# Optimization experiments

Measured on AMD Instinct MI355X. Metric: run time of the kernel, lower is better.

## Reference

```python
import jax, jax.numpy as jnp
import numpy as np

B, V, H = 128, 50257, 2048   # batch, vocab, history length
NEG_INF = jnp.float32(-jnp.inf)
TEMP_MIN = 1e-5


def setup_inputs() -> dict:
    key = jax.random.key(0)
    k1, k2, k3 = jax.random.split(key, 3)
    logits = jax.random.normal(k1, (B, V), jnp.float32) * 4.0
    previous_tokens = jax.random.randint(k2, (B, H), 0, V)
    # uniform noise for the exponential-race (Gumbel-max) draw; strictly positive
    u = jax.random.uniform(k3, (B, V), jnp.float32, minval=1e-10, maxval=1.0)
    return {
        "logits": logits,
        "previous_tokens": previous_tokens,
        "u": u,
        "top_p": jnp.full((1,), 0.9, jnp.float32),
        "repetition_penalty": jnp.full((1,), 1.35, jnp.float32),
        "temperature": jnp.full((1,), 0.7, jnp.float32),
        "top_k": 50,
    }


def _logits_to_probs(logits, previous_tokens, temperature, top_k, top_p, repetition_penalty):
    b = jnp.arange(logits.shape[0])[:, None]  # [B,1] row index for scatters
    # repetition penalty: gather history scores, shrink, scatter back
    score = jnp.take_along_axis(logits, previous_tokens, axis=1)          # [B,H]
    score = jnp.where(score < 0, score * repetition_penalty, score / repetition_penalty)
    logits = logits.at[b, previous_tokens].set(score)                     # [B,V]
    # nucleus (top-p) filtering via descending sort + cumulative softmax
    order = jnp.argsort(-logits, axis=-1)                                 # [B,V]
    sorted_logits = jnp.take_along_axis(logits, order, axis=1)
    cum_probs = jnp.cumsum(jax.nn.softmax(sorted_logits, axis=-1), axis=-1)
    remove_sorted = cum_probs > top_p
    remove_sorted = remove_sorted.at[:, 0].set(False)                     # keep best token
    # scatter removal mask back to vocab order (order is a permutation)
    remove = jnp.zeros_like(remove_sorted).at[b, order].set(remove_sorted)
    logits = jnp.where(remove, NEG_INF, logits)
    # temperature + top-k pivot filter
    logits = logits / jnp.maximum(temperature, TEMP_MIN)
    v = jax.lax.top_k(logits, top_k)[0]                                   # [B,top_k]
    pivot = v[:, -1:]
    logits = jnp.where(logits < pivot, NEG_INF, logits)
    return jax.nn.softmax(logits, axis=-1)


def reference(logits, previous_tokens, u, top_p, repetition_penalty, temperature, top_k):
    previous_tokens = previous_tokens.astype(jnp.int32)
    probs = _logits_to_probs(logits, previous_tokens, temperature, top_k, top_p,
                             repetition_penalty)
    # multinomial_sample_one_no_sync: exponential race argmax(probs / Exp(1))
    q = -jnp.log(u)
    idx_next = jnp.argmax(probs / q, axis=-1, keepdims=True).astype(jnp.int32)
    return idx_next, probs
```

## Files before the change

kernel.cpp:

```cpp
#include <hip/hip_runtime.h>
#include <cfloat>
#include <cmath>
#include <cstdint>

#define VV 50257
#define NT 1024
#define NBUCK 4096
#define CAP 1024
#define BITW ((VV + 31) / 32)
#define NW (NT / 64)

__device__ __forceinline__ unsigned fmono(float f) {
    unsigned b = __float_as_uint(f);
    return b ^ (((int)b < 0) ? 0xFFFFFFFFu : 0x80000000u);
}

__global__ __launch_bounds__(NT) void pp_fused(
    const float* __restrict__ logits, const int* __restrict__ prev,
    const float* __restrict__ u, const float* __restrict__ toppp,
    const float* __restrict__ rpp, const float* __restrict__ tempp,
    const int* __restrict__ topkp, float* __restrict__ out_idx,
    float* __restrict__ out_probs, int Hp)
{
    __shared__ unsigned bitmap[BITW];
    __shared__ unsigned hist[NBUCK];
    __shared__ float cand_v[CAP];
    __shared__ int   cand_i[CAP];
    __shared__ float red_m[NW], red_s[NW];
    __shared__ unsigned wtot[NW];
    __shared__ float tv[64];
    __shared__ int   ti[64];
    __shared__ float sM, sS;
    __shared__ int sT, sCnt;

    const int row = blockIdx.x;
    const int tid = threadIdx.x;
    const int lane = tid & 63;
    const int wid = tid >> 6;
    const float rp = rpp[0];
    const float inv_rp = 1.0f / rp;

    for (int i = tid; i < BITW; i += NT) bitmap[i] = 0u;
    for (int i = tid; i < NBUCK; i += NT) hist[i] = 0u;
    if (tid == 0) { sT = 0; sCnt = 0; }
    if (tid < 64) { tv[tid] = -FLT_MAX; ti[tid] = 0x7FFFFFFF; }
    __syncthreads();

    const int* prow = prev + (size_t)row * Hp;
    for (int i = tid; i < Hp; i += NT) {
        int t = prow[i];
        atomicOr(&bitmap[t >> 5], 1u << (t & 31));
    }
    __syncthreads();

    const float* lrow = logits + (size_t)row * VV;
    float* orow = out_probs + (size_t)row * VV;
    const int pad = (4 - (row & 3)) & 3;
    const int n4 = (VV - pad) >> 2;
    const int tail0 = pad + 4 * n4;
    const float4* lrow4 = (const float4*)(lrow + pad);
    float4* orow4 = (float4*)(orow + pad);

    float m = -FLT_MAX;
    if (tid < pad) {
        float l = lrow[tid];
        if ((bitmap[tid >> 5] >> (tid & 31)) & 1u) l = (l < 0.f) ? l * rp : l * inv_rp;
        atomicAdd(&hist[fmono(l) >> 20], 1u);
        m = fmaxf(m, l);
    }
    #pragma unroll 4
    for (int k = tid; k < n4; k += NT) {
        float4 v = lrow4[k];
        const int base = pad + 4 * k;
        float e[4] = {v.x, v.y, v.z, v.w};
        #pragma unroll
        for (int j = 0; j < 4; ++j) {
            int i = base + j;
            float l = e[j];
            if ((bitmap[i >> 5] >> (i & 31)) & 1u) l = (l < 0.f) ? l * rp : l * inv_rp;
            atomicAdd(&hist[fmono(l) >> 20], 1u);
            m = fmaxf(m, l);
        }
    }
    for (int i = tail0 + tid; i < VV; i += NT) {
        float l = lrow[i];
        if ((bitmap[i >> 5] >> (i & 31)) & 1u) l = (l < 0.f) ? l * rp : l * inv_rp;
        atomicAdd(&hist[fmono(l) >> 20], 1u);
        m = fmaxf(m, l);
    }

    if (tid < pad) orow[tid] = 0.0f;
    const float4 z4 = make_float4(0.f, 0.f, 0.f, 0.f);
    for (int k = tid; k < n4; k += NT) orow4[k] = z4;
    for (int i = tail0 + tid; i < VV; i += NT) orow[i] = 0.0f;

    #pragma unroll
    for (int off = 32; off; off >>= 1) m = fmaxf(m, __shfl_down(m, off));
    if (lane == 0) red_m[wid] = m;
    __syncthreads();
    if (tid == 0) {
        float M = red_m[0];
        for (int w = 1; w < NW; ++w) M = fmaxf(M, red_m[w]);
        sM = M;
    }

    unsigned c = hist[tid * 4] + hist[tid * 4 + 1] + hist[tid * 4 + 2] + hist[tid * 4 + 3];
    unsigned v = c;
    #pragma unroll
    for (int off = 1; off < 64; off <<= 1) {
        unsigned o = __shfl_down(v, off);
        if (lane + off < 64) v += o;
    }
    if (lane == 0) wtot[wid] = v;
    __syncthreads();
    unsigned add = 0;
    for (int w = wid + 1; w < NW; ++w) add += wtot[w];
    const unsigned mySuf = v + add;
    const unsigned sufExcl = mySuf - c;
    if (mySuf >= 64u && sufExcl < 64u) {
        unsigned above = sufExcl;
        for (int b = tid * 4 + 3; b >= tid * 4; --b) {
            above += hist[b];
            if (above >= 64u) { sT = b; break; }
        }
    }
    __syncthreads();
    const unsigned T = (unsigned)sT;
    const float M = sM;

    float s = 0.0f;
    if (tid < pad) {
        float l = lrow[tid];
        if ((bitmap[tid >> 5] >> (tid & 31)) & 1u) l = (l < 0.f) ? l * rp : l * inv_rp;
        s += __expf(l - M);
        if ((fmono(l) >> 20) >= T) {
            int p = atomicAdd(&sCnt, 1);
            if (p < CAP) { cand_v[p] = l; cand_i[p] = tid; }
        }
    }
    #pragma unroll 2
    for (int k = tid; k < n4; k += NT) {
        float4 vv = lrow4[k];
        const int base = pad + 4 * k;
        float e[4] = {vv.x, vv.y, vv.z, vv.w};
        #pragma unroll
        for (int j = 0; j < 4; ++j) {
            int i = base + j;
            float l = e[j];
            if ((bitmap[i >> 5] >> (i & 31)) & 1u) l = (l < 0.f) ? l * rp : l * inv_rp;
            s += __expf(l - M);
            if ((fmono(l) >> 20) >= T) {
                int p = atomicAdd(&sCnt, 1);
                if (p < CAP) { cand_v[p] = l; cand_i[p] = i; }
            }
        }
    }
    for (int i = tail0 + tid; i < VV; i += NT) {
        float l = lrow[i];
        if ((bitmap[i >> 5] >> (i & 31)) & 1u) l = (l < 0.f) ? l * rp : l * inv_rp;
        s += __expf(l - M);
        if ((fmono(l) >> 20) >= T) {
            int p = atomicAdd(&sCnt, 1);
            if (p < CAP) { cand_v[p] = l; cand_i[p] = i; }
        }
    }
    #pragma unroll
    for (int off = 32; off; off >>= 1) s += __shfl_down(s, off);
    if (lane == 0) red_s[wid] = s;
    __syncthreads();
    if (tid == 0) {
        float Ss = red_s[0];
        for (int w = 1; w < NW; ++w) Ss += red_s[w];
        sS = Ss;
    }
    const int cnt = min(sCnt, CAP);

    if (tid < cnt) {
        float vi = cand_v[tid]; int ii = cand_i[tid];
        int r = 0;
        for (int j = 0; j < cnt; ++j) {
            float vj = cand_v[j]; int ij = cand_i[j];
            r += (int)((vj > vi) || (vj == vi && ij < ii));
        }
        if (r < 64) { tv[r] = vi; ti[r] = ii; }
    }
    __syncthreads();

    if (tid < 64) {
        const float top_p = toppp[0];
        const float temp = tempp[0];
        int K = topkp[0]; K = min(max(K, 1), 64);
        const float Ssum = sS;
        float vl = tv[lane];
        int ci = ti[lane];
        bool val = (vl > -FLT_MAX);
        bool act = (lane < K) && val;
        float e = act ? expf(vl - M) / Ssum : 0.0f;
        float cum = e;
        #pragma unroll
        for (int off = 1; off < 64; off <<= 1) {
            float pv = __shfl_up(cum, off);
            if (lane >= off) cum += pv;
        }
        unsigned long long bal = __ballot(act && (cum <= top_p));
        int n = (int)__popcll(bal);
        if (n < 1) n = 1;
        const float v0 = tv[0];
        const float invT = 1.0f / fmaxf(temp, 1e-5f);
        bool keep = (lane < n) && val;
        float w = keep ? expf((vl - v0) * invT) : 0.0f;
        float Z = w;
        #pragma unroll
        for (int off = 32; off; off >>= 1) Z += __shfl_xor(Z, off);
        float p = keep ? (w / Z) : 0.0f;
        if (keep) orow[ci] = p;
        float ratio = -1.0f;
        if (keep) ratio = p / (-logf(u[(size_t)row * VV + ci]));
        int bi = keep ? ci : 0x7FFFFFFF;
        #pragma unroll
        for (int off = 32; off; off >>= 1) {
            float orat = __shfl_xor(ratio, off);
            int oidx = __shfl_xor(bi, off);
            if (orat > ratio || (orat == ratio && oidx < bi)) { ratio = orat; bi = oidx; }
        }
        if (lane == 0) out_idx[row] = (float)bi;
    }
}

extern "C" void kernel_launch(void* const* d_in, const int* in_sizes, int n_in,
                              void* d_out, int out_size, void* d_ws, size_t ws_size,
                              hipStream_t stream) {
    const float* logits = (const float*)d_in[0];
    const int*   prev   = (const int*)d_in[1];
    const float* u      = (const float*)d_in[2];
    const float* topp   = (const float*)d_in[3];
    const float* rp     = (const float*)d_in[4];
    const float* temp   = (const float*)d_in[5];
    const int*   topk   = (const int*)d_in[6];

    const int B  = in_sizes[0] / VV;
    const int Hp = in_sizes[1] / B;

    float* out = (float*)d_out;
    pp_fused<<<B, NT, 0, stream>>>(
        logits, prev, u, topp, rp, temp, topk, out, out + B, Hp);
}
```

Baseline: 33.08 us.

## Split each row across four blocks and merge candidates in a second kernel

The single fused kernel with one block per row becomes two kernels. The first runs SPLITS=4 blocks per row, each handling a vocab chunk. Each chunk block builds its own histogram and candidate list, keeps loaded values in registers instead of re-reading logits in the second pass, and writes a partial max, sum and candidates to workspace. The second kernel merges the partial softmax stats, ranks the combined candidates and does top-p/top-k/sampling. This targets low occupancy (only 128 blocks on a many-CU GPU) at the cost of an extra launch and global round trips for candidates.

```diff
diff --git a/kernel.cpp b/kernel.cpp
--- a/kernel.cpp
+++ b/kernel.cpp
@@ -4,95 +4,104 @@
 #include <cstdint>
 
 #define VV 50257
-#define NT 1024
+#define SPLITS 4
+#define CHUNKA 12568
+#define BMW ((CHUNKA + 31) / 32)
 #define NBUCK 4096
-#define CAP 1024
-#define BITW ((VV + 31) / 32)
-#define NW (NT / 64)
+#define CAPC 256
+#define K1T 512
+#define K2T 512
+#define NJ 7
+#define NW1 (K1T / 64)
 
 __device__ __forceinline__ unsigned fmono(float f) {
     unsigned b = __float_as_uint(f);
     return b ^ (((int)b < 0) ? 0xFFFFFFFFu : 0x80000000u);
 }
 
-__global__ __launch_bounds__(NT) void pp_fused(
+__global__ __launch_bounds__(K1T) void pp_k1(
     const float* __restrict__ logits, const int* __restrict__ prev,
-    const float* __restrict__ u, const float* __restrict__ toppp,
-    const float* __restrict__ rpp, const float* __restrict__ tempp,
-    const int* __restrict__ topkp, float* __restrict__ out_idx,
-    float* __restrict__ out_probs, int Hp)
+    const float* __restrict__ rpp,
+    float* __restrict__ pm, float* __restrict__ ps,
+    float* __restrict__ gcv, int* __restrict__ gci, int* __restrict__ gcnt,
+    float* __restrict__ out_probs, int Hp, int capc)
 {
-    __shared__ unsigned bitmap[BITW];
+    const int sp = blockIdx.x, row = blockIdx.y;
+    const int tid = threadIdx.x, lane = tid & 63, wid = tid >> 6;
+    const int c0 = sp * CHUNKA;
+    const int c1 = min(VV, c0 + CHUNKA);
+    const int len = c1 - c0;
+    const float rp = rpp[0], inv_rp = 1.0f / rp;
+
+    __shared__ unsigned bm[BMW];
     __shared__ unsigned hist[NBUCK];
-    __shared__ float cand_v[CAP];
-    __shared__ int   cand_i[CAP];
-    __shared__ float red_m[NW], red_s[NW];
-    __shared__ unsigned wtot[NW];
-    __shared__ float tv[64];
-    __shared__ int   ti[64];
-    __shared__ float sM, sS;
+    __shared__ float red_m[NW1], red_s[NW1];
+    __shared__ unsigned wtot[NW1];
+    __shared__ float cand_v[CAPC];
+    __shared__ int   cand_i[CAPC];
+    __shared__ float sM;
     __shared__ int sT, sCnt;
 
-    const int row = blockIdx.x;
-    const int tid = threadIdx.x;
-    const int lane = tid & 63;
-    const int wid = tid >> 6;
-    const float rp = rpp[0];
-    const float inv_rp = 1.0f / rp;
-
-    for (int i = tid; i < BITW; i += NT) bitmap[i] = 0u;
-    for (int i = tid; i < NBUCK; i += NT) hist[i] = 0u;
+    for (int i = tid; i < BMW; i += K1T) bm[i] = 0u;
+    for (int i = tid; i < NBUCK; i += K1T) hist[i] = 0u;
     if (tid == 0) { sT = 0; sCnt = 0; }
-    if (tid < 64) { tv[tid] = -FLT_MAX; ti[tid] = 0x7FFFFFFF; }
     __syncthreads();
 
     const int* prow = prev + (size_t)row * Hp;
-    for (int i = tid; i < Hp; i += NT) {
+    for (int i = tid; i < Hp; i += K1T) {
         int t = prow[i];
-        atomicOr(&bitmap[t >> 5], 1u << (t & 31));
+        if (t >= c0 && t < c1) {
+            int o = t - c0;
+            atomicOr(&bm[o >> 5], 1u << (o & 31));
+        }
     }
     __syncthreads();
 
     const float* lrow = logits + (size_t)row * VV;
     float* orow = out_probs + (size_t)row * VV;
     const int pad = (4 - (row & 3)) & 3;
-    const int n4 = (VV - pad) >> 2;
+    const int n4 = (len - pad) >> 2;
     const int tail0 = pad + 4 * n4;
-    const float4* lrow4 = (const float4*)(lrow + pad);
-    float4* orow4 = (float4*)(orow + pad);
-
+    const float4* l4 = (const float4*)(lrow + c0 + pad);
+    float4* o4 = (float4*)(orow + c0 + pad);
+
+    float4 rv[NJ];
     float m = -FLT_MAX;
-    if (tid < pad) {
-        float l = lrow[tid];
-        if ((bitmap[tid >> 5] >> (tid & 31)) & 1u) l = (l < 0.f) ? l * rp : l * inv_rp;
+    for (int o = tid; o < pad; o += K1T) {
+        float l = lrow[c0 + o];
+        if ((bm[o >> 5] >> (o & 31)) & 1u) l = (l < 0.f) ? l * rp : l * inv_rp;
         atomicAdd(&hist[fmono(l) >> 20], 1u);
         m = fmaxf(m, l);
     }
-    #pragma unroll 4
-    for (int k = tid; k < n4; k += NT) {
-        float4 v = lrow4[k];
-        const int base = pad + 4 * k;
-        float e[4] = {v.x, v.y, v.z, v.w};
-        #pragma unroll
-        for (int j = 0; j < 4; ++j) {
-            int i = base + j;
-            float l = e[j];
-            if ((bitmap[i >> 5] >> (i & 31)) & 1u) l = (l < 0.f) ? l * rp : l * inv_rp;
-            atomicAdd(&hist[fmono(l) >> 20], 1u);
-            m = fmaxf(m, l);
-        }
-    }
-    for (int i = tail0 + tid; i < VV; i += NT) {
-        float l = lrow[i];
-        if ((bitmap[i >> 5] >> (i & 31)) & 1u) l = (l < 0.f) ? l * rp : l * inv_rp;
+    #pragma unroll
+    for (int j = 0; j < NJ; ++j) {
+        int k = tid + j * K1T;
+        if (k < n4) {
+            float4 v = l4[k];
+            int ob = pad + 4 * k;
+            float x;
+            x = v.x; if ((bm[(ob+0) >> 5] >> ((ob+0) & 31)) & 1u) x = (x < 0.f) ? x * rp : x * inv_rp;
+            atomicAdd(&hist[fmono(x) >> 20], 1u); m = fmaxf(m, x); v.x = x;
+            x = v.y; if ((bm[(ob+1) >> 5] >> ((ob+1) & 31)) & 1u) x = (x < 0.f) ? x * rp : x * inv_rp;
+            atomicAdd(&hist[fmono(x) >> 20], 1u); m = fmaxf(m, x); v.y = x;
+            x = v.z; if ((bm[(ob+2) >> 5] >> ((ob+2) & 31)) & 1u) x = (x < 0.f) ? x * rp : x * inv_rp;
+            atomicAdd(&hist[fmono(x) >> 20], 1u); m = fmaxf(m, x); v.z = x;
+            x = v.w; if ((bm[(ob+3) >> 5] >> ((ob+3) & 31)) & 1u) x = (x < 0.f) ? x * rp : x * inv_rp;
+            atomicAdd(&hist[fmono(x) >> 20], 1u); m = fmaxf(m, x); v.w = x;
+            rv[j] = v;
+        }
+    }
+    for (int o = tail0 + tid; o < len; o += K1T) {
+        float l = lrow[c0 + o];
+        if ((bm[o >> 5] >> (o & 31)) & 1u) l = (l < 0.f) ? l * rp : l * inv_rp;
         atomicAdd(&hist[fmono(l) >> 20], 1u);
         m = fmaxf(m, l);
     }
 
-    if (tid < pad) orow[tid] = 0.0f;
+    for (int o = tid; o < pad; o += K1T) orow[c0 + o] = 0.f;
     const float4 z4 = make_float4(0.f, 0.f, 0.f, 0.f);
-    for (int k = tid; k < n4; k += NT) orow4[k] = z4;
-    for (int i = tail0 + tid; i < VV; i += NT) orow[i] = 0.0f;
+    for (int k = tid; k < n4; k += K1T) o4[k] = z4;
+    for (int o = tail0 + tid; o < len; o += K1T) orow[c0 + o] = 0.f;
 
     #pragma unroll
     for (int off = 32; off; off >>= 1) m = fmaxf(m, __shfl_down(m, off));
@@ -100,11 +109,13 @@
     __syncthreads();
     if (tid == 0) {
         float M = red_m[0];
-        for (int w = 1; w < NW; ++w) M = fmaxf(M, red_m[w]);
+        for (int w = 1; w < NW1; ++w) M = fmaxf(M, red_m[w]);
         sM = M;
     }
 
-    unsigned c = hist[tid * 4] + hist[tid * 4 + 1] + hist[tid * 4 + 2] + hist[tid * 4 + 3];
+    unsigned c = 0;
+    #pragma unroll
+    for (int j = 0; j < 8; ++j) c += hist[tid * 8 + j];
     unsigned v = c;
     #pragma unroll
     for (int off = 1; off < 64; off <<= 1) {
@@ -114,12 +125,12 @@
     if (lane == 0) wtot[wid] = v;
     __syncthreads();
     unsigned add = 0;
-    for (int w = wid + 1; w < NW; ++w) add += wtot[w];
+    for (int w = wid + 1; w < NW1; ++w) add += wtot[w];
     const unsigned mySuf = v + add;
     const unsigned sufExcl = mySuf - c;
     if (mySuf >= 64u && sufExcl < 64u) {
         unsigned above = sufExcl;
-        for (int b = tid * 4 + 3; b >= tid * 4; --b) {
+        for (int b = tid * 8 + 7; b >= tid * 8; --b) {
             above += hist[b];
             if (above >= 64u) { sT = b; break; }
         }
@@ -127,59 +138,110 @@
     __syncthreads();
     const unsigned T = (unsigned)sT;
     const float M = sM;
+    const int cmax = min(capc, CAPC);
 
     float s = 0.0f;
-    if (tid < pad) {
-        float l = lrow[tid];
-        if ((bitmap[tid >> 5] >> (tid & 31)) & 1u) l = (l < 0.f) ? l * rp : l * inv_rp;
+    for (int o = tid; o < pad; o += K1T) {
+        float l = lrow[c0 + o];
+        if ((bm[o >> 5] >> (o & 31)) & 1u) l = (l < 0.f) ? l * rp : l * inv_rp;
         s += __expf(l - M);
         if ((fmono(l) >> 20) >= T) {
             int p = atomicAdd(&sCnt, 1);
-            if (p < CAP) { cand_v[p] = l; cand_i[p] = tid; }
-        }
-    }
-    #pragma unroll 2
-    for (int k = tid; k < n4; k += NT) {
-        float4 vv = lrow4[k];
-        const int base = pad + 4 * k;
-        float e[4] = {vv.x, vv.y, vv.z, vv.w};
-        #pragma unroll
-        for (int j = 0; j < 4; ++j) {
-            int i = base + j;
-            float l = e[j];
-            if ((bitmap[i >> 5] >> (i & 31)) & 1u) l = (l < 0.f) ? l * rp : l * inv_rp;
-            s += __expf(l - M);
-            if ((fmono(l) >> 20) >= T) {
-                int p = atomicAdd(&sCnt, 1);
-                if (p < CAP) { cand_v[p] = l; cand_i[p] = i; }
-            }
-        }
-    }
-    for (int i = tail0 + tid; i < VV; i += NT) {
-        float l = lrow[i];
-        if ((bitmap[i >> 5] >> (i & 31)) & 1u) l = (l < 0.f) ? l * rp : l * inv_rp;
+            if (p < cmax) { cand_v[p] = l; cand_i[p] = c0 + o; }
+        }
+    }
+    #pragma unroll
+    for (int j = 0; j < NJ; ++j) {
+        int k = tid + j * K1T;
+        if (k < n4) {
+            float4 vv = rv[j];
+            int gi = c0 + pad + 4 * k;
+            s += __expf(vv.x - M);
+            if ((fmono(vv.x) >> 20) >= T) { int p = atomicAdd(&sCnt, 1); if (p < cmax) { cand_v[p] = vv.x; cand_i[p] = gi + 0; } }
+            s += __expf(vv.y - M);
+            if ((fmono(vv.y) >> 20) >= T) { int p = atomicAdd(&sCnt, 1); if (p < cmax) { cand_v[p] = vv.y; cand_i[p] = gi + 1; } }
+            s += __expf(vv.z - M);
+            if ((fmono(vv.z) >> 20) >= T) { int p = atomicAdd(&sCnt, 1); if (p < cmax) { cand_v[p] = vv.z; cand_i[p] = gi + 2; } }
+            s += __expf(vv.w - M);
+            if ((fmono(vv.w) >> 20) >= T) { int p = atomicAdd(&sCnt, 1); if (p < cmax) { cand_v[p] = vv.w; cand_i[p] = gi + 3; } }
+        }
+    }
+    for (int o = tail0 + tid; o < len; o += K1T) {
+        float l = lrow[c0 + o];
+        if ((bm[o >> 5] >> (o & 31)) & 1u) l = (l < 0.f) ? l * rp : l * inv_rp;
         s += __expf(l - M);
         if ((fmono(l) >> 20) >= T) {
             int p = atomicAdd(&sCnt, 1);
-            if (p < CAP) { cand_v[p] = l; cand_i[p] = i; }
+            if (p < cmax) { cand_v[p] = l; cand_i[p] = c0 + o; }
         }
     }
     #pragma unroll
     for (int off = 32; off; off >>= 1) s += __shfl_down(s, off);
     if (lane == 0) red_s[wid] = s;
     __syncthreads();
+
+    const int slot = row * SPLITS + sp;
     if (tid == 0) {
         float Ss = red_s[0];
-        for (int w = 1; w < NW; ++w) Ss += red_s[w];
-        sS = Ss;
-    }
-    const int cnt = min(sCnt, CAP);
-
-    if (tid < cnt) {
-        float vi = cand_v[tid]; int ii = cand_i[tid];
+        for (int w = 1; w < NW1; ++w) Ss += red_s[w];
+        pm[slot] = M;
+        ps[slot] = Ss;
+        gcnt[slot] = min(sCnt, cmax);
+    }
+    const int cnt = min(sCnt, cmax);
+    for (int t = tid; t < cnt; t += K1T) {
+        gcv[(size_t)slot * capc + t] = cand_v[t];
+        gci[(size_t)slot * capc + t] = cand_i[t];
+    }
+}
+
+__global__ __launch_bounds__(K2T) void pp_k2(
+    const float* __restrict__ u, const float* __restrict__ toppp,
+    const float* __restrict__ tempp, const int* __restrict__ topkp,
+    const float* __restrict__ pm, const float* __restrict__ ps,
+    const float* __restrict__ gcv, const int* __restrict__ gci,
+    const int* __restrict__ gcnt,
+    float* __restrict__ out_idx, float* __restrict__ out_probs, int capc)
+{
+    const int row = blockIdx.x, tid = threadIdx.x;
+    __shared__ float cv[SPLITS * CAPC];
+    __shared__ int   cidx[SPLITS * CAPC];
+    __shared__ float tv[64];
+    __shared__ int   ti[64];
+    __shared__ float sM, sS;
+
+    int c4[SPLITS], off[SPLITS];
+    int tot = 0;
+    #pragma unroll
+    for (int j = 0; j < SPLITS; ++j) {
+        c4[j] = gcnt[row * SPLITS + j];
+        off[j] = tot;
+        tot += c4[j];
+    }
+    #pragma unroll
+    for (int j = 0; j < SPLITS; ++j)
+        for (int i = tid; i < c4[j]; i += K2T) {
+            cv[off[j] + i]   = gcv[(size_t)(row * SPLITS + j) * capc + i];
+            cidx[off[j] + i] = gci[(size_t)(row * SPLITS + j) * capc + i];
+        }
+    if (tid < 64) { tv[tid] = -FLT_MAX; ti[tid] = 0x7FFFFFFF; }
+    if (tid == 0) {
+        float M = pm[row * SPLITS], S = ps[row * SPLITS];
+        for (int j = 1; j < SPLITS; ++j) {
+            float m2 = pm[row * SPLITS + j], s2 = ps[row * SPLITS + j];
+            float nm = fmaxf(M, m2);
+            S = S * __expf(M - nm) + s2 * __expf(m2 - nm);
+            M = nm;
+        }
+        sM = M; sS = S;
+    }
+    __syncthreads();
+
+    for (int t = tid; t < tot; t += K2T) {
+        float vi = cv[t]; int ii = cidx[t];
         int r = 0;
-        for (int j = 0; j < cnt; ++j) {
-            float vj = cand_v[j]; int ij = cand_i[j];
+        for (int j2 = 0; j2 < tot; ++j2) {
+            float vj = cv[j2]; int ij = cidx[j2];
             r += (int)((vj > vi) || (vj == vi && ij < ii));
         }
         if (r < 64) { tv[r] = vi; ti[r] = ii; }
@@ -187,10 +249,11 @@
     __syncthreads();
 
     if (tid < 64) {
+        const int lane = tid;
         const float top_p = toppp[0];
         const float temp = tempp[0];
         int K = topkp[0]; K = min(max(K, 1), 64);
-        const float Ssum = sS;
+        const float M = sM, Ssum = sS;
         float vl = tv[lane];
         int ci = ti[lane];
         bool val = (vl > -FLT_MAX);
@@ -198,9 +261,9 @@
         float e = act ? expf(vl - M) / Ssum : 0.0f;
         float cum = e;
         #pragma unroll
-        for (int off = 1; off < 64; off <<= 1) {
-            float pv = __shfl_up(cum, off);
-            if (lane >= off) cum += pv;
+        for (int off2 = 1; off2 < 64; off2 <<= 1) {
+            float pv = __shfl_up(cum, off2);
+            if (lane >= off2) cum += pv;
         }
         unsigned long long bal = __ballot(act && (cum <= top_p));
         int n = (int)__popcll(bal);
@@ -211,16 +274,16 @@
         float w = keep ? expf((vl - v0) * invT) : 0.0f;
         float Z = w;
         #pragma unroll
-        for (int off = 32; off; off >>= 1) Z += __shfl_xor(Z, off);
+        for (int off2 = 32; off2; off2 >>= 1) Z += __shfl_xor(Z, off2);
         float p = keep ? (w / Z) : 0.0f;
-        if (keep) orow[ci] = p;
+        if (keep) out_probs[(size_t)row * VV + ci] = p;
         float ratio = -1.0f;
         if (keep) ratio = p / (-logf(u[(size_t)row * VV + ci]));
         int bi = keep ? ci : 0x7FFFFFFF;
         #pragma unroll
-        for (int off = 32; off; off >>= 1) {
-            float orat = __shfl_xor(ratio, off);
-            int oidx = __shfl_xor(bi, off);
+        for (int off2 = 32; off2; off2 >>= 1) {
+            float orat = __shfl_xor(ratio, off2);
+            int oidx = __shfl_xor(bi, off2);
             if (orat > ratio || (orat == ratio && oidx < bi)) { ratio = orat; bi = oidx; }
         }
         if (lane == 0) out_idx[row] = (float)bi;
@@ -241,7 +304,21 @@
     const int B  = in_sizes[0] / VV;
     const int Hp = in_sizes[1] / B;
 
+    char* ws = (char*)d_ws;
+    int*   gcnt = (int*)ws;
+    float* pm   = (float*)(ws + 8192);
+    float* ps   = pm + (size_t)B * SPLITS;
+    char*  cbase = ws + 16384;
+    long long avail = (long long)ws_size - 16384;
+    int capc = (int)(avail / (8LL * B * SPLITS));
+    if (capc > CAPC) capc = CAPC;
+    if (capc < 64) capc = 64;
+    float* gcv = (float*)cbase;
+    int*   gci = (int*)(cbase + (size_t)B * SPLITS * capc * 4);
+
     float* out = (float*)d_out;
-    pp_fused<<<B, NT, 0, stream>>>(
-        logits, prev, u, topp, rp, temp, topk, out, out + B, Hp);
+    pp_k1<<<dim3(SPLITS, B), K1T, 0, stream>>>(
+        logits, prev, rp, pm, ps, gcv, gci, gcnt, out + B, Hp, capc);
+    pp_k2<<<B, K2T, 0, stream>>>(
+        u, topp, temp, topk, pm, ps, gcv, gci, gcnt, out, out + B, capc);
 }
```

After: 63.96 us. +93.4%, slower.
